# Kernel tuning notes

Hardware: AMD Instinct MI355X
Metric: run time of the kernel (lower is better)

## Reference

```python
import jax, jax.numpy as jnp
import numpy as np
import math

D = 1280      # embed_dim ('650M')
H = 20        # n_head
DH = D // H   # d_hidden = 64
DFF = 4 * D   # r_ff = 4
LN_EPS = 1e-5


def layer_norm(x, gamma, beta):
    mu = jnp.mean(x, axis=-1, keepdims=True)
    var = jnp.var(x, axis=-1, keepdims=True)
    return (x - mu) * jax.lax.rsqrt(var + LN_EPS) * gamma + beta


def setup_inputs() -> dict:
    key = jax.random.key(0)
    ks = jax.random.split(key, 16)
    B, L = 2, 2048
    x = jax.random.normal(ks[0], (B, L, D), dtype=jnp.float32)
    y = jax.random.normal(ks[1], (B, L, D), dtype=jnp.float32)  # dm_embeds (unused by module)
    s_qkv = 1.0 / math.sqrt(D)
    Wq = jax.random.uniform(ks[2], (D, D), jnp.float32, -s_qkv, s_qkv)
    Wk = jax.random.uniform(ks[3], (D, D), jnp.float32, -s_qkv, s_qkv)
    Wv = jax.random.uniform(ks[4], (D, D), jnp.float32, -s_qkv, s_qkv)
    Wo = jax.random.uniform(ks[5], (D, D), jnp.float32, -s_qkv, s_qkv)
    bo = jnp.zeros((D,), jnp.float32)
    W1 = jax.random.normal(ks[6], (D, DFF), jnp.float32) * math.sqrt(2.0 / D)  # kaiming
    b1 = jnp.zeros((DFF,), jnp.float32)
    W2 = jax.random.uniform(ks[7], (DFF, D), jnp.float32, -1.0 / math.sqrt(DFF), 1.0 / math.sqrt(DFF))
    b2 = jnp.zeros((D,), jnp.float32)
    g1 = jnp.ones((D,), jnp.float32); be1 = jnp.zeros((D,), jnp.float32)
    g2 = jnp.ones((D,), jnp.float32); be2 = jnp.zeros((D,), jnp.float32)
    return dict(x=x, y=y, Wq=Wq, Wk=Wk, Wv=Wv, Wo=Wo, bo=bo,
                W1=W1, b1=b1, W2=W2, b2=b2, g1=g1, be1=be1, g2=g2, be2=be2)


def reference(x, y, Wq, Wk, Wv, Wo, bo, W1, b1, W2, b2, g1, be1, g2, be2):
    B, L, _ = x.shape
    scaling = 1.0 / math.sqrt(DH)
    # --- pre-norm self-attention ---
    xn = layer_norm(x, g1, be1)
    q = (xn @ Wq).reshape(B, L, H, DH) * scaling
    k = (xn @ Wk).reshape(B, L, H, DH)
    v = (xn @ Wv).reshape(B, L, H, DH)
    scores = jnp.einsum('bqhd,bkhd->bhqk', q, k)
    attn = jax.nn.softmax(scores, axis=-1)
    o = jnp.einsum('bhqk,bkhd->bqhd', attn, v).reshape(B, L, D)
    x = x + (o @ Wo + bo)
    # --- pre-norm FFN ---
    xn = layer_norm(x, g2, be2)
    h = jax.nn.relu(xn @ W1 + b1)
    x = x + (h @ W2 + b2)
    return x
```

## Files before the change

kernel.cpp:

```cpp
#include <hip/hip_runtime.h>

typedef short bf16x8 __attribute__((ext_vector_type(8)));
typedef short bf16x4 __attribute__((ext_vector_type(4)));
typedef float f32x4 __attribute__((ext_vector_type(4)));
typedef unsigned short u16;

#define GL16(g, l) __builtin_amdgcn_global_load_lds( \
    (const __attribute__((address_space(1))) void*)(g), \
    (__attribute__((address_space(3))) void*)(l), 16, 0, 0)

__device__ __forceinline__ u16 f2bf(float f) {
  union { float f; unsigned u; } v; v.f = f;
  return (u16)((v.u + 0x7fffu + ((v.u >> 16) & 1u)) >> 16);
}

__device__ __forceinline__ float exp2_(float x) {
#if __has_builtin(__builtin_amdgcn_exp2f)
  return __builtin_amdgcn_exp2f(x);
#else
  return __expf(x * 0.69314718056f);
#endif
}

__device__ __forceinline__ unsigned cvtpk(float a, float b) {
  unsigned r;
  asm("v_cvt_pk_bf16_f32 %0, %1, %2" : "=v"(r) : "v"(a), "v"(b));
  return r;
}

__global__ __launch_bounds__(256) void ln_kernel(
    const float* __restrict__ x, const float* __restrict__ g,
    const float* __restrict__ b, u16* __restrict__ out) {
  const int row = blockIdx.x, tid = threadIdx.x;
  const float4* xr = (const float4*)(x + (size_t)row * 1280);
  float4 v1 = xr[tid];
  float4 v2 = make_float4(0.f, 0.f, 0.f, 0.f);
  if (tid < 64) v2 = xr[256 + tid];
  float s = v1.x + v1.y + v1.z + v1.w + v2.x + v2.y + v2.z + v2.w;
  float q = v1.x * v1.x + v1.y * v1.y + v1.z * v1.z + v1.w * v1.w +
            v2.x * v2.x + v2.y * v2.y + v2.z * v2.z + v2.w * v2.w;
#pragma unroll
  for (int off = 32; off >= 1; off >>= 1) {
    s += __shfl_xor(s, off);
    q += __shfl_xor(q, off);
  }
  __shared__ float sm[8];
  if ((tid & 63) == 0) { sm[tid >> 6] = s; sm[4 + (tid >> 6)] = q; }
  __syncthreads();
  s = sm[0] + sm[1] + sm[2] + sm[3];
  q = sm[4] + sm[5] + sm[6] + sm[7];
  const float mean = s * (1.0f / 1280.0f);
  const float rstd = rsqrtf(q * (1.0f / 1280.0f) - mean * mean + 1e-5f);
  const float4* gr = (const float4*)g;
  const float4* br = (const float4*)b;
  u16* orow = out + (size_t)row * 1280;
  {
    float4 gg = gr[tid], bb = br[tid];
    ushort4 o;
    o.x = f2bf((v1.x - mean) * rstd * gg.x + bb.x);
    o.y = f2bf((v1.y - mean) * rstd * gg.y + bb.y);
    o.z = f2bf((v1.z - mean) * rstd * gg.z + bb.z);
    o.w = f2bf((v1.w - mean) * rstd * gg.w + bb.w);
    *(ushort4*)&orow[tid * 4] = o;
  }
  if (tid < 64) {
    float4 gg = gr[256 + tid], bb = br[256 + tid];
    ushort4 o;
    o.x = f2bf((v2.x - mean) * rstd * gg.x + bb.x);
    o.y = f2bf((v2.y - mean) * rstd * gg.y + bb.y);
    o.z = f2bf((v2.z - mean) * rstd * gg.z + bb.z);
    o.w = f2bf((v2.w - mean) * rstd * gg.w + bb.w);
    *(ushort4*)&orow[(256 + tid) * 4] = o;
  }
}

__global__ __launch_bounds__(256) void tconv_kernel(
    const float* __restrict__ src, u16* __restrict__ dst,
    int rows, int cols, float scale) {
  __shared__ float t[64][33];
  const int tid = threadIdx.x;
  const size_t c0 = (size_t)blockIdx.x * 64, r0 = (size_t)blockIdx.y * 32;
  const int ty = tid >> 4, col4 = tid & 15;
#pragma unroll
  for (int i = 0; i < 2; ++i) {
    const int row = ty + i * 16;
    float4 v = *(const float4*)&src[(r0 + row) * cols + c0 + col4 * 4];
    t[col4 * 4 + 0][row] = v.x;
    t[col4 * 4 + 1][row] = v.y;
    t[col4 * 4 + 2][row] = v.z;
    t[col4 * 4 + 3][row] = v.w;
  }
  __syncthreads();
  const int c = tid >> 2, rb = (tid & 3) * 8;
  ushort4 o1, o2;
  o1.x = f2bf(t[c][rb + 0] * scale); o1.y = f2bf(t[c][rb + 1] * scale);
  o1.z = f2bf(t[c][rb + 2] * scale); o1.w = f2bf(t[c][rb + 3] * scale);
  o2.x = f2bf(t[c][rb + 4] * scale); o2.y = f2bf(t[c][rb + 5] * scale);
  o2.z = f2bf(t[c][rb + 6] * scale); o2.w = f2bf(t[c][rb + 7] * scale);
  u16* d = &dst[(c0 + c) * rows + r0 + rb];
  *(ushort4*)d = o1;
  *(ushort4*)(d + 4) = o2;
}

__global__ __launch_bounds__(256) void tconv3_kernel(
    const float* __restrict__ s0, const float* __restrict__ s1,
    const float* __restrict__ s2, u16* __restrict__ dst, float scale0) {
  __shared__ float t[64][33];
  const int tid = threadIdx.x, z = blockIdx.z;
  const float* src = (z == 0) ? s0 : ((z == 1) ? s1 : s2);
  const float scale = (z == 0) ? scale0 : 1.0f;
  u16* d0 = dst + (size_t)z * 1280 * 1280;
  const size_t c0 = (size_t)blockIdx.x * 64, r0 = (size_t)blockIdx.y * 32;
  const int ty = tid >> 4, col4 = tid & 15;
#pragma unroll
  for (int i = 0; i < 2; ++i) {
    const int row = ty + i * 16;
    float4 v = *(const float4*)&src[(r0 + row) * 1280 + c0 + col4 * 4];
    t[col4 * 4 + 0][row] = v.x;
    t[col4 * 4 + 1][row] = v.y;
    t[col4 * 4 + 2][row] = v.z;
    t[col4 * 4 + 3][row] = v.w;
  }
  __syncthreads();
  const int c = tid >> 2, rb = (tid & 3) * 8;
  ushort4 o1, o2;
  o1.x = f2bf(t[c][rb + 0] * scale); o1.y = f2bf(t[c][rb + 1] * scale);
  o1.z = f2bf(t[c][rb + 2] * scale); o1.w = f2bf(t[c][rb + 3] * scale);
  o2.x = f2bf(t[c][rb + 4] * scale); o2.y = f2bf(t[c][rb + 5] * scale);
  o2.z = f2bf(t[c][rb + 6] * scale); o2.w = f2bf(t[c][rb + 7] * scale);
  u16* d = &d0[(c0 + c) * 1280 + r0 + rb];
  *(ushort4*)d = o1;
  *(ushort4*)(d + 4) = o2;
}

__global__ __launch_bounds__(256) void vtrans_kernel(const u16* __restrict__ qkv,
                                                     u16* __restrict__ vt) {
  __shared__ u16 t[64][65];
  const int tx = threadIdx.x & 63, ty = threadIdx.x >> 6;
  const int t0 = blockIdx.x * 64, bh = blockIdx.y, b = bh / 20, h = bh % 20;
  const u16* src = qkv + (size_t)b * 2048 * 3840 + 2560 + h * 64;
  for (int i = ty; i < 64; i += 4) t[i][tx] = src[(size_t)(t0 + i) * 3840 + tx];
  __syncthreads();
  u16* dst = vt + (size_t)bh * 64 * 2048 + t0;
  for (int i = ty; i < 64; i += 4) dst[(size_t)i * 2048 + tx] = t[tx][i];
}

__global__ __launch_bounds__(256) void initadd_kernel(
    const float* __restrict__ src, const float* __restrict__ bias,
    float* __restrict__ out) {
  const size_t i = (size_t)blockIdx.x * 256 + threadIdx.x;
  float4 v = ((const float4*)src)[i];
  float4 b = ((const float4*)bias)[i % 320];
  v.x += b.x; v.y += b.y; v.z += b.z; v.w += b.w;
  ((float4*)out)[i] = v;
}

template <int EPI>
__device__ __forceinline__ void gemm_body(
    const u16* __restrict__ A, const u16* __restrict__ BT,
    const float* __restrict__ bias, void* __restrict__ out,
    int M, int N, int K, int kSteps) {
  __shared__ __attribute__((aligned(16))) u16 Als[3][128 * 32];
  __shared__ __attribute__((aligned(16))) u16 Bls[3][128 * 32];
  const int tid = threadIdx.x;
  const int w = tid >> 6, lane = tid & 63;
  const int lo = lane & 15, hi = lane >> 4;
  const int wm = w >> 1, wn = w & 1;
  const int gx = gridDim.x, gxy = gx * gridDim.y;
  const int nwg = gxy * gridDim.z;
  int s = blockIdx.x + gx * blockIdx.y + gxy * blockIdx.z;
  s = (s & 7) * (nwg >> 3) + (s >> 3);
  const int bz = s / gxy; s -= bz * gxy;
  const int by = s / gx;  const int bx = s - by * gx;
  const size_t m0 = (size_t)by * 128, n0 = (size_t)bx * 128;
  const int kt0 = bz * kSteps;
  f32x4 acc[4][4] = {};
  const int srow = w * 32 + (lane >> 2);
  const int scol = ((lane & 3) ^ ((lane >> 3) & 3)) * 8;
  const int rsw = (lo >> 1) & 3;
#define STAGE(buf, kt)                                                        \
  do {                                                                        \
    const size_t kb = (size_t)(kt) * 32 + scol;                               \
    GL16(&A[(m0 + srow) * K + kb],       &Als[buf][(w * 2 + 0) * 512]);       \
    GL16(&A[(m0 + srow + 16) * K + kb],  &Als[buf][(w * 2 + 1) * 512]);       \
    GL16(&BT[(n0 + srow) * K + kb],      &Bls[buf][(w * 2 + 0) * 512]);       \
    GL16(&BT[(n0 + srow + 16) * K + kb], &Bls[buf][(w * 2 + 1) * 512]);       \
  } while (0)
  STAGE(0, kt0 + 0);
  STAGE(1, kt0 + 1);
  int cur = 0;
  for (int t = 0; t < kSteps; ++t) {
    if (t + 1 < kSteps) asm volatile("s_waitcnt vmcnt(4)" ::: "memory");
    else                asm volatile("s_waitcnt vmcnt(0)" ::: "memory");
    __builtin_amdgcn_s_barrier();
    __builtin_amdgcn_sched_barrier(0);
    const int nxt = (cur == 0) ? 2 : cur - 1;
    if (t + 2 < kSteps) STAGE(nxt, kt0 + t + 2);
    bf16x8 af[4], bfr[4];
#pragma unroll
    for (int mi = 0; mi < 4; ++mi)
      af[mi] = *(const bf16x8*)&Als[cur][(wm * 64 + mi * 16 + lo) * 32 + ((hi ^ rsw) * 8)];
#pragma unroll
    for (int ni = 0; ni < 4; ++ni)
      bfr[ni] = *(const bf16x8*)&Bls[cur][(wn * 64 + ni * 16 + lo) * 32 + ((hi ^ rsw) * 8)];
#pragma unroll
    for (int mi = 0; mi < 4; ++mi)
#pragma unroll
      for (int ni = 0; ni < 4; ++ni)
        acc[mi][ni] = __builtin_amdgcn_mfma_f32_16x16x32_bf16(
            af[mi], bfr[ni], acc[mi][ni], 0, 0, 0);
    cur = (cur == 2) ? 0 : cur + 1;
  }
#undef STAGE
#pragma unroll
  for (int ni = 0; ni < 4; ++ni) {
    const size_t col = n0 + wn * 64 + ni * 16 + lo;
    const float bv = (EPI == 1) ? bias[col] : 0.0f;
#pragma unroll
    for (int mi = 0; mi < 4; ++mi) {
      const size_t rb = m0 + wm * 64 + mi * 16 + hi * 4;
#pragma unroll
      for (int r = 0; r < 4; ++r) {
        const size_t idx = (rb + r) * N + col;
        float v = acc[mi][ni][r];
        if (EPI == 0) {
          ((u16*)out)[idx] = f2bf(v);
        } else if (EPI == 1) {
          v += bv;
          v = fmaxf(v, 0.0f);
          ((u16*)out)[idx] = f2bf(v);
        } else {
          atomicAdd(&((float*)out)[idx], v);
        }
      }
    }
  }
}

__global__ __launch_bounds__(256, 3) void gemm_oproj(
    const u16* __restrict__ A, const u16* __restrict__ BT,
    void* __restrict__ out, int M, int N, int K, int kSteps) {
  gemm_body<3>(A, BT, nullptr, out, M, N, K, kSteps);
}

template <int EPI>
__device__ __forceinline__ void gemm8v2_body(
    const u16* __restrict__ A, const u16* __restrict__ BT,
    const float* __restrict__ bias, void* __restrict__ out,
    int M, int N, int K, int nt) {
  __shared__ __attribute__((aligned(16))) u16 Als[2][2][128 * 64];
  __shared__ __attribute__((aligned(16))) u16 Bls[2][2][128 * 64];
  const int tid = threadIdx.x;
  const int w = tid >> 6, lane = tid & 63;
  const int lo = lane & 15, hi = lane >> 4;
  const int wm = w >> 2, wn = w & 3;
  const int gx = gridDim.x, gxy = gx * gridDim.y;
  const int nwg = gxy * gridDim.z;
  int s = blockIdx.x + gx * blockIdx.y + gxy * blockIdx.z;
  s = (s & 7) * (nwg >> 3) + (s >> 3);
  const int bz = s / gxy; s -= bz * gxy;
  const int by = s / gx;  const int bx = s - by * gx;
  const size_t m0 = (size_t)by * 256, n0 = (size_t)bx * 256;
  const int kt0 = bz * nt;
  f32x4 acc[8][4] = {};
  const int srowo = lane >> 3;
  const int gcol = ((lane & 7) ^ (lane >> 3)) * 8;
  const int rsw = lo & 7;
#define STG(dstbuf, srcp, rbase, kt)                                          \
  do {                                                                        \
    const size_t kb = (size_t)(kt) * 64 + gcol;                               \
    GL16(&srcp[(rbase + w * 16 + srowo) * K + kb], &dstbuf[(w * 16) * 64]);   \
    GL16(&srcp[(rbase + w * 16 + 8 + srowo) * K + kb],                        \
         &dstbuf[(w * 16 + 8) * 64]);                                         \
  } while (0)
#define BAR()   __builtin_amdgcn_s_barrier()
#define SB0()   __builtin_amdgcn_sched_barrier(0)
#define LGKM0() asm volatile("s_waitcnt lgkmcnt(0)" ::: "memory")
#define VM6()   asm volatile("s_waitcnt vmcnt(6)" ::: "memory")
#define VM0()   asm volatile("s_waitcnt vmcnt(0)" ::: "memory")
  STG(Als[0][0], A,  m0,       kt0 + 0);
  STG(Bls[0][0], BT, n0,       kt0 + 0);
  STG(Bls[1][0], BT, n0 + 128, kt0 + 0);
  STG(Als[1][0], A,  m0 + 128, kt0 + 0);
  for (int t = 0; t < nt; ++t) {
    const int sl = t & 1, sn = sl ^ 1;
    const bool pf = (t + 1 < nt);
    bf16x8 a0[4][2], a1[4][2], b0[2][2], b1[2][2];
    if (pf) { STG(Als[0][sn], A, m0, kt0 + t + 1); SB0(); VM6(); }
    else    { VM0(); }
    BAR(); SB0();
#pragma unroll
    for (int mi = 0; mi < 4; ++mi)
#pragma unroll
      for (int ks = 0; ks < 2; ++ks)
        a0[mi][ks] = *(const bf16x8*)&Als[0][sl][(wm * 64 + mi * 16 + lo) * 64 +
                                                (((ks * 4 + hi) ^ rsw) * 8)];
#pragma unroll
    for (int ni = 0; ni < 2; ++ni)
#pragma unroll
      for (int ks = 0; ks < 2; ++ks)
        b0[ni][ks] = *(const bf16x8*)&Bls[0][sl][(wn * 32 + ni * 16 + lo) * 64 +
                                                (((ks * 4 + hi) ^ rsw) * 8)];
    LGKM0(); SB0();
    __builtin_amdgcn_s_setprio(1);
#pragma unroll
    for (int mi = 0; mi < 4; ++mi)
#pragma unroll
      for (int ni = 0; ni < 2; ++ni)
#pragma unroll
        for (int ks = 0; ks < 2; ++ks)
          acc[mi][ni] = __builtin_amdgcn_mfma_f32_16x16x32_bf16(
              a0[mi][ks], b0[ni][ks], acc[mi][ni], 0, 0, 0);
    __builtin_amdgcn_s_setprio(0);
    if (pf) { STG(Bls[0][sn], BT, n0, kt0 + t + 1); SB0(); VM6(); }
    else    { VM0(); }
    BAR(); SB0();
#pragma unroll
    for (int ni = 0; ni < 2; ++ni)
#pragma unroll
      for (int ks = 0; ks < 2; ++ks)
        b1[ni][ks] = *(const bf16x8*)&Bls[1][sl][(wn * 32 + ni * 16 + lo) * 64 +
                                                (((ks * 4 + hi) ^ rsw) * 8)];
    LGKM0(); SB0();
    __builtin_amdgcn_s_setprio(1);
#pragma unroll
    for (int mi = 0; mi < 4; ++mi)
#pragma unroll
      for (int ni = 0; ni < 2; ++ni)
#pragma unroll
        for (int ks = 0; ks < 2; ++ks)
          acc[mi][ni + 2] = __builtin_amdgcn_mfma_f32_16x16x32_bf16(
              a0[mi][ks], b1[ni][ks], acc[mi][ni + 2], 0, 0, 0);
    __builtin_amdgcn_s_setprio(0);
    if (pf) { STG(Bls[1][sn], BT, n0 + 128, kt0 + t + 1); SB0(); VM6(); }
    else    { VM0(); }
    BAR(); SB0();
#pragma unroll
    for (int mi = 0; mi < 4; ++mi)
#pragma unroll
      for (int ks = 0; ks < 2; ++ks)
        a1[mi][ks] = *(const bf16x8*)&Als[1][sl][(wm * 64 + mi * 16 + lo) * 64 +
                                                (((ks * 4 + hi) ^ rsw) * 8)];
    LGKM0(); SB0();
    __builtin_amdgcn_s_setprio(1);
#pragma unroll
    for (int mi = 0; mi < 4; ++mi)
#pragma unroll
      for (int ni = 0; ni < 2; ++ni)
#pragma unroll
        for (int ks = 0; ks < 2; ++ks)
          acc[mi + 4][ni] = __builtin_amdgcn_mfma_f32_16x16x32_bf16(
              a1[mi][ks], b0[ni][ks], acc[mi + 4][ni], 0, 0, 0);
    __builtin_amdgcn_s_setprio(0);
    if (pf) STG(Als[1][sn], A, m0 + 128, kt0 + t + 1);
    SB0();
    __builtin_amdgcn_s_setprio(1);
#pragma unroll
    for (int mi = 0; mi < 4; ++mi)
#pragma unroll
      for (int ni = 0; ni < 2; ++ni)
#pragma unroll
        for (int ks = 0; ks < 2; ++ks)
          acc[mi + 4][ni + 2] = __builtin_amdgcn_mfma_f32_16x16x32_bf16(
              a1[mi][ks], b1[ni][ks], acc[mi + 4][ni + 2], 0, 0, 0);
    __builtin_amdgcn_s_setprio(0);
  }
#undef STG
#undef BAR
#undef SB0
#undef LGKM0
#undef VM6
#undef VM0
#pragma unroll
  for (int ni = 0; ni < 4; ++ni) {
    const int ncol = (ni < 2) ? (wn * 32 + ni * 16) : (128 + wn * 32 + (ni - 2) * 16);
    const size_t col = n0 + ncol + lo;
    const float bv = (EPI == 1) ? bias[col] : 0.0f;
#pragma unroll
    for (int mi = 0; mi < 8; ++mi) {
      const int mrow = (mi < 4) ? (wm * 64 + mi * 16) : (128 + wm * 64 + (mi - 4) * 16);
      const size_t rb = m0 + mrow + hi * 4;
#pragma unroll
      for (int r = 0; r < 4; ++r) {
        const size_t idx = (rb + r) * N + col;
        float v = acc[mi][ni][r];
        if (EPI == 0) {
          ((u16*)out)[idx] = f2bf(v);
        } else if (EPI == 1) {
          v += bv;
          v = fmaxf(v, 0.0f);
          ((u16*)out)[idx] = f2bf(v);
        } else {
          atomicAdd(&((float*)out)[idx], v);
        }
      }
    }
  }
}

__global__ __launch_bounds__(512, 2) void gemm_qkv8(
    const u16* __restrict__ A, const u16* __restrict__ BT,
    void* __restrict__ out, int M, int N, int K, int nt) {
  gemm8v2_body<0>(A, BT, nullptr, out, M, N, K, nt);
}
__global__ __launch_bounds__(512, 2) void gemm_ffn18(
    const u16* __restrict__ A, const u16* __restrict__ BT,
    const float* __restrict__ bias, void* __restrict__ out,
    int M, int N, int K, int nt) {
  gemm8v2_body<1>(A, BT, bias, out, M, N, K, nt);
}
__global__ __launch_bounds__(512, 2) void gemm_ffn28(
    const u16* __restrict__ A, const u16* __restrict__ BT,
    void* __restrict__ out, int M, int N, int K, int nt) {
  gemm8v2_body<3>(A, BT, nullptr, out, M, N, K, nt);
}

__global__ __launch_bounds__(512) void attn_kernel(
    const u16* __restrict__ qkv, const u16* __restrict__ vt,
    u16* __restrict__ aout) {
  __shared__ __attribute__((aligned(16))) u16 Klds[64 * 64];
  __shared__ __attribute__((aligned(16))) u16 Vlds[64 * 64];
  __shared__ __attribute__((aligned(16))) u16 Plds[8][16][72];
  const int tid = threadIdx.x;
  const int w = tid >> 6, lane = tid & 63;
  const int lo = lane & 15, hi = lane >> 4;
  const int bh = blockIdx.x, qt = blockIdx.y;
  const int b = bh / 20, h = bh % 20;
  const size_t qrow = (size_t)b * 2048 + qt * 128 + w * 16 + lo;
  bf16x8 qf[2];
  qf[0] = *(const bf16x8*)&qkv[qrow * 3840 + h * 64 + hi * 8];
  qf[1] = *(const bf16x8*)&qkv[qrow * 3840 + h * 64 + 32 + hi * 8];
  float m_i = -1e30f, l_i = 0.0f;
  f32x4 accO[4] = {};
  const int srow = lane >> 3;
  const int scol = ((lane & 7) ^ srow) * 8;
  const u16* kbase = qkv + (size_t)b * 2048 * 3840 + 1280 + h * 64;
  const u16* vbase = vt + (size_t)bh * 64 * 2048;
  for (int kt = 0; kt < 32; ++kt) {
    {
      const int row = w * 8 + srow;
      GL16(kbase + (size_t)(kt * 64 + row) * 3840 + scol, &Klds[w * 512]);
      GL16(vbase + (size_t)row * 2048 + kt * 64 + scol, &Vlds[w * 512]);
    }
    __syncthreads();
    f32x4 s4[4] = {};
    __builtin_amdgcn_s_setprio(1);
#pragma unroll
    for (int st = 0; st < 4; ++st) {
      const int row = st * 16 + lo;
      const int sw = (row & 7) << 3;
#pragma unroll
      for (int ks = 0; ks < 2; ++ks) {
        bf16x8 a = *(const bf16x8*)&Klds[row * 64 + ((ks * 32 + hi * 8) ^ sw)];
        s4[st] = __builtin_amdgcn_mfma_f32_16x16x32_bf16(a, qf[ks], s4[st], 0, 0, 0);
      }
    }
    __builtin_amdgcn_s_setprio(0);
    float tm = fmaxf(fmaxf(fmaxf(s4[0][0], s4[0][1]), fmaxf(s4[0][2], s4[0][3])),
                     fmaxf(fmaxf(s4[1][0], s4[1][1]), fmaxf(s4[1][2], s4[1][3])));
    tm = fmaxf(tm, fmaxf(fmaxf(fmaxf(s4[2][0], s4[2][1]), fmaxf(s4[2][2], s4[2][3])),
                         fmaxf(fmaxf(s4[3][0], s4[3][1]), fmaxf(s4[3][2], s4[3][3]))));
    tm = fmaxf(tm, __shfl_xor(tm, 16));
    tm = fmaxf(tm, __shfl_xor(tm, 32));
    if (!__all(tm <= m_i + 8.0f)) {
      const float mnew = fmaxf(m_i, tm);
      const float corr = exp2_(m_i - mnew);
      m_i = mnew;
      l_i *= corr;
      float cr[4];
#pragma unroll
      for (int r = 0; r < 4; ++r) cr[r] = __shfl(corr, hi * 4 + r);
#pragma unroll
      for (int d = 0; d < 4; ++d)
#pragma unroll
        for (int r = 0; r < 4; ++r) accO[d][r] *= cr[r];
    }
#pragma unroll
    for (int st = 0; st < 4; ++st)
#pragma unroll
      for (int r = 0; r < 4; ++r) {
        const float p = exp2_(s4[st][r] - m_i);
        s4[st][r] = p;
        l_i += p;
      }
#pragma unroll
    for (int st = 0; st < 4; ++st) {
      uint2 pk;
      pk.x = cvtpk(s4[st][0], s4[st][1]);
      pk.y = cvtpk(s4[st][2], s4[st][3]);
      *(uint2*)&Plds[w][lo][st * 16 + hi * 4] = pk;
    }
    asm volatile("s_waitcnt lgkmcnt(0)" ::: "memory");
    __builtin_amdgcn_sched_barrier(0);
    __builtin_amdgcn_s_setprio(1);
#pragma unroll
    for (int ks = 0; ks < 2; ++ks) {
      bf16x8 pa = *(const bf16x8*)&Plds[w][lo][ks * 32 + hi * 8];
#pragma unroll
      for (int d = 0; d < 4; ++d) {
        const int row = d * 16 + lo;
        bf16x8 vb = *(const bf16x8*)
            &Vlds[row * 64 + ((ks * 32 + hi * 8) ^ ((row & 7) << 3))];
        accO[d] = __builtin_amdgcn_mfma_f32_16x16x32_bf16(pa, vb, accO[d], 0, 0, 0);
      }
    }
    __builtin_amdgcn_s_setprio(0);
    __syncthreads();
  }
  l_i += __shfl_xor(l_i, 16);
  l_i += __shfl_xor(l_i, 32);
  float linv[4];
#pragma unroll
  for (int r = 0; r < 4; ++r) linv[r] = 1.0f / __shfl(l_i, hi * 4 + r);
  const size_t orow0 = (size_t)b * 2048 + qt * 128 + w * 16 + hi * 4;
#pragma unroll
  for (int d = 0; d < 4; ++d)
#pragma unroll
    for (int r = 0; r < 4; ++r)
      aout[(orow0 + r) * 1280 + h * 64 + d * 16 + lo] =
          f2bf(accO[d][r] * linv[r]);
}

extern "C" void kernel_launch(void* const* d_in, const int* in_sizes, int n_in,
                              void* d_out, int out_size, void* d_ws, size_t ws_size,
                              hipStream_t stream) {
  const float* x   = (const float*)d_in[0];
  const float* Wq  = (const float*)d_in[2];
  const float* Wk  = (const float*)d_in[3];
  const float* Wv  = (const float*)d_in[4];
  const float* Wo  = (const float*)d_in[5];
  const float* bo  = (const float*)d_in[6];
  const float* W1  = (const float*)d_in[7];
  const float* b1  = (const float*)d_in[8];
  const float* W2  = (const float*)d_in[9];
  const float* b2  = (const float*)d_in[10];
  const float* g1  = (const float*)d_in[11];
  const float* be1 = (const float*)d_in[12];
  const float* g2  = (const float*)d_in[13];
  const float* be2 = (const float*)d_in[14];

  u16* xn   = (u16*)d_ws;
  u16* Wqkv = xn + (size_t)4096 * 1280;
  u16* WoT  = Wqkv + (size_t)3840 * 1280;
  u16* W1T  = WoT + (size_t)1280 * 1280;
  u16* W2T  = W1T + (size_t)5120 * 1280;
  u16* aOut = W2T + (size_t)1280 * 5120;
  float* x1 = (float*)(aOut + (size_t)4096 * 1280);
  u16* qkvb = (u16*)(x1 + (size_t)4096 * 1280);
  u16* vtb  = qkvb + (size_t)4096 * 3840;
  u16* hbuf = qkvb;

  const float qscale = 0.125f * 1.4426950408889634f;
  ln_kernel<<<4096, 256, 0, stream>>>(x, g1, be1, xn);
  tconv3_kernel<<<dim3(20, 40, 3), 256, 0, stream>>>(Wq, Wk, Wv, Wqkv, qscale);
  tconv_kernel<<<dim3(20, 40), 256, 0, stream>>>(Wo, WoT, 1280, 1280, 1.0f);
  tconv_kernel<<<dim3(80, 40), 256, 0, stream>>>(W1, W1T, 1280, 5120, 1.0f);
  tconv_kernel<<<dim3(20, 160), 256, 0, stream>>>(W2, W2T, 5120, 1280, 1.0f);
  gemm_qkv8<<<dim3(15, 16), 512, 0, stream>>>(xn, Wqkv, qkvb, 4096, 3840, 1280, 20);
  vtrans_kernel<<<dim3(32, 40), 256, 0, stream>>>(qkvb, vtb);
  attn_kernel<<<dim3(40, 16), 512, 0, stream>>>(qkvb, vtb, aOut);
  initadd_kernel<<<5120, 256, 0, stream>>>(x, bo, x1);
  gemm_oproj<<<dim3(10, 32, 2), 256, 0, stream>>>(aOut, WoT, x1, 4096, 1280, 1280, 20);
  ln_kernel<<<4096, 256, 0, stream>>>(x1, g2, be2, xn);
  gemm_ffn18<<<dim3(20, 16), 512, 0, stream>>>(xn, W1T, b1, hbuf, 4096, 5120, 1280, 20);
  initadd_kernel<<<5120, 256, 0, stream>>>(x1, b2, (float*)d_out);
  gemm_ffn28<<<dim3(5, 16, 4), 512, 0, stream>>>(hbuf, W2T, d_out, 4096, 1280, 5120, 20);
  (void)in_sizes; (void)n_in; (void)out_size; (void)ws_size;
}
```

Before: 440.3 us.

## Fuse residual/bias init into out-proj epilogue and retile FFN GEMMs to 128x64

Removes both initadd kernels. The out-projection GEMM now runs without split-K and writes x1 = acc + bo + x directly, plus d_out = x1 + b2 as the base for the FFN2 atomic accumulation. A new 128x64-tile GEMM with BK=64 and three-stage LDS buffering replaces the 256x256-style 8-wave kernels for FFN1 and FFN2, with FFN2 split-K changed from 4 to 2. This saves launches and memory passes but gives smaller tiles, less reuse per block, and a different occupancy.

```diff
diff --git a/kernel.cpp b/kernel.cpp
--- a/kernel.cpp
+++ b/kernel.cpp
@@ -145,23 +145,14 @@
   for (int i = ty; i < 64; i += 4) dst[(size_t)i * 2048 + tx] = t[tx][i];
 }
 
-__global__ __launch_bounds__(256) void initadd_kernel(
-    const float* __restrict__ src, const float* __restrict__ bias,
-    float* __restrict__ out) {
-  const size_t i = (size_t)blockIdx.x * 256 + threadIdx.x;
-  float4 v = ((const float4*)src)[i];
-  float4 b = ((const float4*)bias)[i % 320];
-  v.x += b.x; v.y += b.y; v.z += b.z; v.w += b.w;
-  ((float4*)out)[i] = v;
-}
-
 template <int EPI>
-__device__ __forceinline__ void gemm_body(
+__device__ __forceinline__ void gemm64_body(
     const u16* __restrict__ A, const u16* __restrict__ BT,
-    const float* __restrict__ bias, void* __restrict__ out,
-    int M, int N, int K, int kSteps) {
-  __shared__ __attribute__((aligned(16))) u16 Als[3][128 * 32];
-  __shared__ __attribute__((aligned(16))) u16 Bls[3][128 * 32];
+    const float* __restrict__ bias, const float* __restrict__ res,
+    const float* __restrict__ bias2, float* __restrict__ out2,
+    void* __restrict__ out, int M, int N, int K, int nt) {
+  __shared__ __attribute__((aligned(16))) u16 Als[3][128 * 64];
+  __shared__ __attribute__((aligned(16))) u16 Bls[3][64 * 64];
   const int tid = threadIdx.x;
   const int w = tid >> 6, lane = tid & 63;
   const int lo = lane & 15, hi = lane >> 4;
@@ -172,50 +163,65 @@
   s = (s & 7) * (nwg >> 3) + (s >> 3);
   const int bz = s / gxy; s -= bz * gxy;
   const int by = s / gx;  const int bx = s - by * gx;
-  const size_t m0 = (size_t)by * 128, n0 = (size_t)bx * 128;
-  const int kt0 = bz * kSteps;
-  f32x4 acc[4][4] = {};
-  const int srow = w * 32 + (lane >> 2);
-  const int scol = ((lane & 3) ^ ((lane >> 3) & 3)) * 8;
-  const int rsw = (lo >> 1) & 3;
+  const size_t m0 = (size_t)by * 128, n0 = (size_t)bx * 64;
+  const int kt0 = bz * nt;
+  f32x4 acc[4][2] = {};
+  const int srowo = lane >> 3;
+  const int gcol = ((lane & 7) ^ (lane >> 3)) * 8;
+  const int rsw = lo & 7;
 #define STAGE(buf, kt)                                                        \
   do {                                                                        \
-    const size_t kb = (size_t)(kt) * 32 + scol;                               \
-    GL16(&A[(m0 + srow) * K + kb],       &Als[buf][(w * 2 + 0) * 512]);       \
-    GL16(&A[(m0 + srow + 16) * K + kb],  &Als[buf][(w * 2 + 1) * 512]);       \
-    GL16(&BT[(n0 + srow) * K + kb],      &Bls[buf][(w * 2 + 0) * 512]);       \
-    GL16(&BT[(n0 + srow + 16) * K + kb], &Bls[buf][(w * 2 + 1) * 512]);       \
+    const size_t kb = (size_t)(kt) * 64 + gcol;                               \
+    _Pragma("unroll")                                                         \
+    for (int i = 0; i < 4; ++i) {                                             \
+      const int ch = w * 4 + i;                                               \
+      GL16(&A[(m0 + ch * 8 + srowo) * K + kb], &Als[buf][ch * 512]);          \
+    }                                                                         \
+    _Pragma("unroll")                                                         \
+    for (int i = 0; i < 2; ++i) {                                             \
+      const int ch = w * 2 + i;                                               \
+      GL16(&BT[(n0 + ch * 8 + srowo) * K + kb], &Bls[buf][ch * 512]);         \
+    }                                                                         \
   } while (0)
   STAGE(0, kt0 + 0);
   STAGE(1, kt0 + 1);
   int cur = 0;
-  for (int t = 0; t < kSteps; ++t) {
-    if (t + 1 < kSteps) asm volatile("s_waitcnt vmcnt(4)" ::: "memory");
-    else                asm volatile("s_waitcnt vmcnt(0)" ::: "memory");
+  for (int t = 0; t < nt; ++t) {
+    if (t + 1 < nt) asm volatile("s_waitcnt vmcnt(6)" ::: "memory");
+    else            asm volatile("s_waitcnt vmcnt(0)" ::: "memory");
     __builtin_amdgcn_s_barrier();
     __builtin_amdgcn_sched_barrier(0);
     const int nxt = (cur == 0) ? 2 : cur - 1;
-    if (t + 2 < kSteps) STAGE(nxt, kt0 + t + 2);
-    bf16x8 af[4], bfr[4];
-#pragma unroll
-    for (int mi = 0; mi < 4; ++mi)
-      af[mi] = *(const bf16x8*)&Als[cur][(wm * 64 + mi * 16 + lo) * 32 + ((hi ^ rsw) * 8)];
-#pragma unroll
-    for (int ni = 0; ni < 4; ++ni)
-      bfr[ni] = *(const bf16x8*)&Bls[cur][(wn * 64 + ni * 16 + lo) * 32 + ((hi ^ rsw) * 8)];
-#pragma unroll
-    for (int mi = 0; mi < 4; ++mi)
-#pragma unroll
-      for (int ni = 0; ni < 4; ++ni)
-        acc[mi][ni] = __builtin_amdgcn_mfma_f32_16x16x32_bf16(
-            af[mi], bfr[ni], acc[mi][ni], 0, 0, 0);
+    if (t + 2 < nt) STAGE(nxt, kt0 + t + 2);
+    bf16x8 af[4][2], bfr[2][2];
+#pragma unroll
+    for (int mi = 0; mi < 4; ++mi)
+#pragma unroll
+      for (int kk = 0; kk < 2; ++kk)
+        af[mi][kk] = *(const bf16x8*)&Als[cur][(wm * 64 + mi * 16 + lo) * 64 +
+                                              (((kk * 4 + hi) ^ rsw) * 8)];
+#pragma unroll
+    for (int ni = 0; ni < 2; ++ni)
+#pragma unroll
+      for (int kk = 0; kk < 2; ++kk)
+        bfr[ni][kk] = *(const bf16x8*)&Bls[cur][(wn * 32 + ni * 16 + lo) * 64 +
+                                               (((kk * 4 + hi) ^ rsw) * 8)];
+#pragma unroll
+    for (int mi = 0; mi < 4; ++mi)
+#pragma unroll
+      for (int ni = 0; ni < 2; ++ni)
+#pragma unroll
+        for (int kk = 0; kk < 2; ++kk)
+          acc[mi][ni] = __builtin_amdgcn_mfma_f32_16x16x32_bf16(
+              af[mi][kk], bfr[ni][kk], acc[mi][ni], 0, 0, 0);
     cur = (cur == 2) ? 0 : cur + 1;
   }
 #undef STAGE
 #pragma unroll
-  for (int ni = 0; ni < 4; ++ni) {
-    const size_t col = n0 + wn * 64 + ni * 16 + lo;
-    const float bv = (EPI == 1) ? bias[col] : 0.0f;
+  for (int ni = 0; ni < 2; ++ni) {
+    const size_t col = n0 + wn * 32 + ni * 16 + lo;
+    const float bv = (EPI == 1 || EPI == 4) ? bias[col] : 0.0f;
+    const float bv2 = (EPI == 4) ? bias2[col] : 0.0f;
 #pragma unroll
     for (int mi = 0; mi < 4; ++mi) {
       const size_t rb = m0 + wm * 64 + mi * 16 + hi * 4;
@@ -223,12 +229,14 @@
       for (int r = 0; r < 4; ++r) {
         const size_t idx = (rb + r) * N + col;
         float v = acc[mi][ni][r];
-        if (EPI == 0) {
-          ((u16*)out)[idx] = f2bf(v);
-        } else if (EPI == 1) {
+        if (EPI == 1) {
           v += bv;
           v = fmaxf(v, 0.0f);
           ((u16*)out)[idx] = f2bf(v);
+        } else if (EPI == 4) {
+          const float v2 = v + bv + res[idx];
+          ((float*)out)[idx] = v2;
+          out2[idx] = v2 + bv2;
         } else {
           atomicAdd(&((float*)out)[idx], v);
         }
@@ -237,10 +245,23 @@
   }
 }
 
-__global__ __launch_bounds__(256, 3) void gemm_oproj(
+__global__ __launch_bounds__(256, 2) void gemm_oproj64(
     const u16* __restrict__ A, const u16* __restrict__ BT,
-    void* __restrict__ out, int M, int N, int K, int kSteps) {
-  gemm_body<3>(A, BT, nullptr, out, M, N, K, kSteps);
+    const float* __restrict__ bias, const float* __restrict__ res,
+    const float* __restrict__ bias2, float* __restrict__ dout,
+    void* __restrict__ out, int M, int N, int K, int nt) {
+  gemm64_body<4>(A, BT, bias, res, bias2, dout, out, M, N, K, nt);
+}
+__global__ __launch_bounds__(256, 2) void gemm_ffn164(
+    const u16* __restrict__ A, const u16* __restrict__ BT,
+    const float* __restrict__ bias, void* __restrict__ out,
+    int M, int N, int K, int nt) {
+  gemm64_body<1>(A, BT, bias, nullptr, nullptr, nullptr, out, M, N, K, nt);
+}
+__global__ __launch_bounds__(256, 2) void gemm_ffn264(
+    const u16* __restrict__ A, const u16* __restrict__ BT,
+    void* __restrict__ out, int M, int N, int K, int nt) {
+  gemm64_body<3>(A, BT, nullptr, nullptr, nullptr, nullptr, out, M, N, K, nt);
 }
 
 template <int EPI>
@@ -375,7 +396,6 @@
   for (int ni = 0; ni < 4; ++ni) {
     const int ncol = (ni < 2) ? (wn * 32 + ni * 16) : (128 + wn * 32 + (ni - 2) * 16);
     const size_t col = n0 + ncol + lo;
-    const float bv = (EPI == 1) ? bias[col] : 0.0f;
 #pragma unroll
     for (int mi = 0; mi < 8; ++mi) {
       const int mrow = (mi < 4) ? (wm * 64 + mi * 16) : (128 + wm * 64 + (mi - 4) * 16);
@@ -383,16 +403,7 @@
 #pragma unroll
       for (int r = 0; r < 4; ++r) {
         const size_t idx = (rb + r) * N + col;
-        float v = acc[mi][ni][r];
-        if (EPI == 0) {
-          ((u16*)out)[idx] = f2bf(v);
-        } else if (EPI == 1) {
-          v += bv;
-          v = fmaxf(v, 0.0f);
-          ((u16*)out)[idx] = f2bf(v);
-        } else {
-          atomicAdd(&((float*)out)[idx], v);
-        }
+        ((u16*)out)[idx] = f2bf(acc[mi][ni][r]);
       }
     }
   }
@@ -402,17 +413,6 @@
     const u16* __restrict__ A, const u16* __restrict__ BT,
     void* __restrict__ out, int M, int N, int K, int nt) {
   gemm8v2_body<0>(A, BT, nullptr, out, M, N, K, nt);
-}
-__global__ __launch_bounds__(512, 2) void gemm_ffn18(
-    const u16* __restrict__ A, const u16* __restrict__ BT,
-    const float* __restrict__ bias, void* __restrict__ out,
-    int M, int N, int K, int nt) {
-  gemm8v2_body<1>(A, BT, bias, out, M, N, K, nt);
-}
-__global__ __launch_bounds__(512, 2) void gemm_ffn28(
-    const u16* __restrict__ A, const u16* __restrict__ BT,
-    void* __restrict__ out, int M, int N, int K, int nt) {
-  gemm8v2_body<3>(A, BT, nullptr, out, M, N, K, nt);
 }
 
 __global__ __launch_bounds__(512) void attn_kernel(
@@ -559,11 +559,11 @@
   gemm_qkv8<<<dim3(15, 16), 512, 0, stream>>>(xn, Wqkv, qkvb, 4096, 3840, 1280, 20);
   vtrans_kernel<<<dim3(32, 40), 256, 0, stream>>>(qkvb, vtb);
   attn_kernel<<<dim3(40, 16), 512, 0, stream>>>(qkvb, vtb, aOut);
-  initadd_kernel<<<5120, 256, 0, stream>>>(x, bo, x1);
-  gemm_oproj<<<dim3(10, 32, 2), 256, 0, stream>>>(aOut, WoT, x1, 4096, 1280, 1280, 20);
+  gemm_oproj64<<<dim3(20, 32), 256, 0, stream>>>(aOut, WoT, bo, x, b2,
+                                                 (float*)d_out, x1,
+                                                 4096, 1280, 1280, 20);
   ln_kernel<<<4096, 256, 0, stream>>>(x1, g2, be2, xn);
-  gemm_ffn18<<<dim3(20, 16), 512, 0, stream>>>(xn, W1T, b1, hbuf, 4096, 5120, 1280, 20);
-  initadd_kernel<<<5120, 256, 0, stream>>>(x1, b2, (float*)d_out);
-  gemm_ffn28<<<dim3(5, 16, 4), 512, 0, stream>>>(hbuf, W2T, d_out, 4096, 1280, 5120, 20);
+  gemm_ffn164<<<dim3(80, 32), 256, 0, stream>>>(xn, W1T, b1, hbuf, 4096, 5120, 1280, 20);
+  gemm_ffn264<<<dim3(20, 32, 2), 256, 0, stream>>>(hbuf, W2T, d_out, 4096, 1280, 5120, 40);
   (void)in_sizes; (void)n_in; (void)out_size; (void)ws_size;
 }
```

Result: faster. 415.7 us (-5.6%).
